# Kernel tuning notes

Measured on AMD Instinct MI355X. Metric: run time of the kernel, lower is better.

## Reference

```python
import jax, jax.numpy as jnp
import numpy as np

D_MODEL, D_STATE, D_CONV, EXPAND = 1024, 16, 4, 2
D_INNER = EXPAND * D_MODEL
BATCH, SEQLEN = 2, 1024


def setup_inputs() -> dict:
    key = jax.random.key(0)
    ks = jax.random.split(key, 8)
    s = lambda fan: 1.0 / np.sqrt(fan)
    x = jax.random.normal(ks[0], (BATCH, SEQLEN, D_MODEL), jnp.float32)
    in_proj_w = jax.random.normal(ks[1], (2 * D_INNER, D_MODEL), jnp.float32) * s(D_MODEL)
    conv_w = jax.random.normal(ks[2], (D_INNER, D_CONV), jnp.float32) * s(D_CONV)
    conv_b = jax.random.normal(ks[3], (D_INNER,), jnp.float32) * 0.02
    x_proj_w = jax.random.normal(ks[4], (2 * D_STATE + 1, D_INNER), jnp.float32) * s(D_INNER)
    dt_proj_w = jax.random.normal(ks[5], (D_INNER, 1), jnp.float32)
    dt_proj_b = jax.random.normal(ks[6], (D_INNER,), jnp.float32) * 0.02
    A_log = jnp.log(jnp.broadcast_to(jnp.arange(1, D_STATE + 1, dtype=jnp.float32), (D_INNER, D_STATE)))
    D_param = jnp.ones((D_INNER,), jnp.float32)
    out_proj_w = jax.random.normal(ks[7], (D_MODEL, D_INNER), jnp.float32) * s(D_INNER)
    return {"x": x, "in_proj_w": in_proj_w, "conv_w": conv_w, "conv_b": conv_b,
            "x_proj_w": x_proj_w, "dt_proj_w": dt_proj_w, "dt_proj_b": dt_proj_b,
            "A_log": A_log, "D_param": D_param, "out_proj_w": out_proj_w}


def reference(x, in_proj_w, conv_w, conv_b, x_proj_w, dt_proj_w, dt_proj_b, A_log, D_param, out_proj_w):
    B, L, _ = x.shape
    d_inner, d_conv = conv_w.shape
    N = A_log.shape[1]

    # in_proj: [B,L,d_model] -> [B,L,2*d_inner], split into ssm branch and gate
    xz = x @ in_proj_w.T
    x_ssm, z = jnp.split(xz, 2, axis=-1)

    # causal depthwise conv1d (padding d_conv-1 on the left, truncated to L)
    xpad = jnp.pad(x_ssm, ((0, 0), (d_conv - 1, 0), (0, 0)))
    xc = conv_b + sum(conv_w[:, k] * xpad[:, k:k + L, :] for k in range(d_conv))
    xc = jax.nn.silu(xc)

    # selective SSM
    A = -jnp.exp(A_log)                                    # [d_inner, N]
    xp = xc @ x_proj_w.T                                   # [B,L,2N+1]
    dt_r, Bv, Cv = xp[..., :1], xp[..., 1:1 + N], xp[..., 1 + N:]
    dt = jax.nn.softplus(dt_r @ dt_proj_w.T + dt_proj_b)   # [B,L,d_inner]
    dA = jnp.exp(dt[..., None] * A)                        # [B,L,d_inner,N]
    dBx = (dt * xc)[..., None] * Bv[:, :, None, :]         # [B,L,d_inner,N]

    def step(h, inputs):
        dA_t, dBx_t, C_t = inputs                          # [B,D,N],[B,D,N],[B,N]
        h = dA_t * h + dBx_t
        y = jnp.einsum('bdn,bn->bd', h, C_t)
        return h, y

    h0 = jnp.zeros((B, d_inner, N), x.dtype)
    xs = (jnp.moveaxis(dA, 1, 0), jnp.moveaxis(dBx, 1, 0), jnp.moveaxis(Cv, 1, 0))
    _, ys = jax.lax.scan(step, h0, xs)                     # ys: [L,B,d_inner]
    y = jnp.moveaxis(ys, 0, 1) + xc * D_param

    y = y * jax.nn.silu(z)
    return y @ out_proj_w.T
```

## Files before the change

### kernel.cpp

```cpp
#include <hip/hip_runtime.h>
#include <hip/hip_bf16.h>
#include <math.h>

#define B_   2
#define L_   1024
#define DM   1024
#define DI   2048
#define NS   16
#define NPJ  33
#define XPW_STRIDE 64
#define NCH  64
#define CHL  16

typedef __bf16 bf16x8 __attribute__((ext_vector_type(8)));
typedef float  f32x4  __attribute__((ext_vector_type(4)));

__device__ __forceinline__ unsigned short f2bf_rn(float x) {
    union { float f; unsigned u; } a; a.f = x;
    unsigned r = a.u + 0x7fffu + ((a.u >> 16) & 1u);
    return (unsigned short)(r >> 16);
}
__device__ __forceinline__ float bf2f(unsigned short h) {
    union { unsigned u; float f; } a; a.u = ((unsigned)h) << 16;
    return a.f;
}
__device__ __forceinline__ float sigmoidf_(float x) { return 1.f / (1.f + __expf(-x)); }
__device__ __forceinline__ float softplusf_(float x) {
    return x > 20.f ? x : log1pf(__expf(x));
}

#define GLDS(g, l) __builtin_amdgcn_global_load_lds( \
    (__attribute__((address_space(1))) void*)(g),    \
    (__attribute__((address_space(3))) void*)(l), 16, 0, 0)

#define XN4   524288
#define W1N4  1048576
#define W2N4  524288
#define WPN4  32768
__global__ __launch_bounds__(256) void cast_all_kernel(
    const float* __restrict__ x, const float* __restrict__ w1,
    const float* __restrict__ w2, const float* __restrict__ xpw,
    unsigned short* __restrict__ xh, unsigned short* __restrict__ xl,
    unsigned short* __restrict__ w1h, unsigned short* __restrict__ w1l,
    unsigned short* __restrict__ w2h, unsigned short* __restrict__ w2l,
    unsigned short* __restrict__ wph, unsigned short* __restrict__ wpl)
{
    int i = blockIdx.x * 256 + threadIdx.x;
    float4 v;
    ushort4 *dh, *dl;
    int li;
    if (i < XN4) {
        li = i; v = ((const float4*)x)[li];
        dh = (ushort4*)xh; dl = (ushort4*)xl;
    } else if (i < XN4 + W1N4) {
        li = i - XN4; v = ((const float4*)w1)[li];
        dh = (ushort4*)w1h; dl = (ushort4*)w1l;
    } else if (i < XN4 + W1N4 + W2N4) {
        li = i - (XN4 + W1N4); v = ((const float4*)w2)[li];
        dh = (ushort4*)w2h; dl = (ushort4*)w2l;
    } else if (i < XN4 + W1N4 + W2N4 + WPN4) {
        li = i - (XN4 + W1N4 + W2N4);
        int j = li >> 9;
        v = (j < NPJ) ? ((const float4*)xpw)[li] : make_float4(0.f, 0.f, 0.f, 0.f);
        dh = (ushort4*)wph; dl = (ushort4*)wpl;
    } else return;
    ushort4 H, L;
    H.x = f2bf_rn(v.x); L.x = f2bf_rn(v.x - bf2f(H.x));
    H.y = f2bf_rn(v.y); L.y = f2bf_rn(v.y - bf2f(H.y));
    H.z = f2bf_rn(v.z); L.z = f2bf_rn(v.z - bf2f(H.z));
    H.w = f2bf_rn(v.w); L.w = f2bf_rn(v.w - bf2f(H.w));
    dh[li] = H; dl[li] = L;
}

template<int BM, int BN, bool AL, bool ATOMIC>
__global__ __launch_bounds__(256) void gemm3_bt(
    const unsigned short* __restrict__ Ah, const unsigned short* __restrict__ Al,
    const unsigned short* __restrict__ Bh, const unsigned short* __restrict__ Bl,
    float* __restrict__ C, int M, int N, int K, int KC)
{
    constexpr int BK = 64;
    constexpr int FM = BM / 32;
    constexpr int FN = BN / 32;
    __shared__ alignas(16) char sAh[BM * BK * 2];
    __shared__ alignas(16) char sAl[AL ? BM * BK * 2 : 16];
    __shared__ alignas(16) char sBh[BN * BK * 2];
    __shared__ alignas(16) char sBl[BN * BK * 2];

    const int tid  = threadIdx.x;
    const int lane = tid & 63;
    const int wave = tid >> 6;
    const int wm = wave >> 1, wn = wave & 1;
    const int m0 = blockIdx.y * BM, n0 = blockIdx.x * BN;
    const int k0 = blockIdx.z * KC;

    f32x4 acc[FM][FN];
#pragma unroll
    for (int i = 0; i < FM; ++i)
#pragma unroll
        for (int j = 0; j < FN; ++j)
            acc[i][j] = (f32x4){0.f, 0.f, 0.f, 0.f};

    for (int kt = k0; kt < k0 + KC; kt += BK) {
#pragma unroll
        for (int iss = 0; iss < BM / 32; ++iss) {
            int o  = (iss * 256 + tid) * 16;
            int r  = o >> 7;
            int cb = (o & 127) ^ ((r & 7) << 4);
            size_t goff = (size_t)(m0 + r) * K + kt + (cb >> 1);
            GLDS(Ah + goff, sAh + iss * 4096 + wave * 1024);
            if (AL) GLDS(Al + goff, sAl + iss * 4096 + wave * 1024);
        }
#pragma unroll
        for (int iss = 0; iss < BN / 32; ++iss) {
            int o  = (iss * 256 + tid) * 16;
            int r  = o >> 7;
            int cb = (o & 127) ^ ((r & 7) << 4);
            size_t goff = (size_t)(n0 + r) * K + kt + (cb >> 1);
            GLDS(Bh + goff, sBh + iss * 4096 + wave * 1024);
            GLDS(Bl + goff, sBl + iss * 4096 + wave * 1024);
        }
        __syncthreads();

#pragma unroll
        for (int kk = 0; kk < 2; ++kk) {
            const int ke = kk * 32 + (lane >> 4) * 8;
            bf16x8 ah[FM], al[FM], bh[FN], bl[FN];
#pragma unroll
            for (int i = 0; i < FM; ++i) {
                int r = wm * (BM / 2) + i * 16 + (lane & 15);
                int off = (r * 128 + ke * 2) ^ ((r & 7) << 4);
                ah[i] = *(const bf16x8*)(sAh + off);
                if (AL) al[i] = *(const bf16x8*)(sAl + off);
            }
#pragma unroll
            for (int j = 0; j < FN; ++j) {
                int r = wn * (BN / 2) + j * 16 + (lane & 15);
                int off = (r * 128 + ke * 2) ^ ((r & 7) << 4);
                bh[j] = *(const bf16x8*)(sBh + off);
                bl[j] = *(const bf16x8*)(sBl + off);
            }
#pragma unroll
            for (int i = 0; i < FM; ++i)
#pragma unroll
                for (int j = 0; j < FN; ++j) {
                    acc[i][j] = __builtin_amdgcn_mfma_f32_16x16x32_bf16(ah[i], bh[j], acc[i][j], 0, 0, 0);
                    acc[i][j] = __builtin_amdgcn_mfma_f32_16x16x32_bf16(ah[i], bl[j], acc[i][j], 0, 0, 0);
                    if (AL) acc[i][j] = __builtin_amdgcn_mfma_f32_16x16x32_bf16(al[i], bh[j], acc[i][j], 0, 0, 0);
                }
        }
        __syncthreads();
    }

    float* Cz = ATOMIC ? C : (C + (size_t)blockIdx.z * M * N);
#pragma unroll
    for (int i = 0; i < FM; ++i)
#pragma unroll
        for (int j = 0; j < FN; ++j) {
            int row = m0 + wm * (BM / 2) + i * 16 + (lane >> 4) * 4;
            int col = n0 + wn * (BN / 2) + j * 16 + (lane & 15);
            float* p = Cz + (size_t)row * N + col;
#pragma unroll
            for (int q = 0; q < 4; ++q) {
                if (ATOMIC) atomicAdd(p + (size_t)q * N, acc[i][j][q]);
                else        p[(size_t)q * N] = acc[i][j][q];
            }
        }
}

__global__ __launch_bounds__(256) void gemm3_xproj(
    const unsigned short* __restrict__ Ah, const unsigned short* __restrict__ Al,
    const unsigned short* __restrict__ Bh, const unsigned short* __restrict__ Bl,
    float* __restrict__ part)
{
    constexpr int BM = 64, BN = 64, BK = 64, KTOT = 2048, KC = 256;
    __shared__ alignas(16) char sAh[BM * 128];
    __shared__ alignas(16) char sAl[BM * 128];
    __shared__ alignas(16) char sBh[BN * 128];
    __shared__ alignas(16) char sBl[BN * 128];

    const int tid  = threadIdx.x;
    const int lane = tid & 63;
    const int wave = tid >> 6;
    const int wm = wave >> 1, wn = wave & 1;
    const int m0 = blockIdx.y * BM;
    const int kt0 = blockIdx.z * KC;

    f32x4 acc[2][2];
#pragma unroll
    for (int i = 0; i < 2; ++i)
#pragma unroll
        for (int j = 0; j < 2; ++j) acc[i][j] = (f32x4){0.f, 0.f, 0.f, 0.f};

    for (int kt = 0; kt < KC; kt += BK) {
#pragma unroll
        for (int iss = 0; iss < 2; ++iss) {
            int o  = (iss * 256 + tid) * 16;
            int r  = o >> 7;
            int cb = (o & 127) ^ ((r & 7) << 4);
            size_t ga = (size_t)(m0 + r) * KTOT + kt0 + kt + (cb >> 1);
            GLDS(Ah + ga, sAh + iss * 4096 + wave * 1024);
            GLDS(Al + ga, sAl + iss * 4096 + wave * 1024);
            size_t gb = (size_t)r * KTOT + kt0 + kt + (cb >> 1);
            GLDS(Bh + gb, sBh + iss * 4096 + wave * 1024);
            GLDS(Bl + gb, sBl + iss * 4096 + wave * 1024);
        }
        __syncthreads();

#pragma unroll
        for (int kk = 0; kk < 2; ++kk) {
            const int ke = kk * 32 + (lane >> 4) * 8;
            bf16x8 ah[2], al[2], bh[2], bl[2];
#pragma unroll
            for (int i = 0; i < 2; ++i) {
                int r = wm * 32 + i * 16 + (lane & 15);
                int off = (r * 128 + ke * 2) ^ ((r & 7) << 4);
                ah[i] = *(const bf16x8*)(sAh + off);
                al[i] = *(const bf16x8*)(sAl + off);
            }
#pragma unroll
            for (int j = 0; j < 2; ++j) {
                int r = wn * 32 + j * 16 + (lane & 15);
                int off = (r * 128 + ke * 2) ^ ((r & 7) << 4);
                bh[j] = *(const bf16x8*)(sBh + off);
                bl[j] = *(const bf16x8*)(sBl + off);
            }
#pragma unroll
            for (int i = 0; i < 2; ++i)
#pragma unroll
                for (int j = 0; j < 2; ++j) {
                    acc[i][j] = __builtin_amdgcn_mfma_f32_16x16x32_bf16(ah[i], bh[j], acc[i][j], 0, 0, 0);
                    acc[i][j] = __builtin_amdgcn_mfma_f32_16x16x32_bf16(ah[i], bl[j], acc[i][j], 0, 0, 0);
                    acc[i][j] = __builtin_amdgcn_mfma_f32_16x16x32_bf16(al[i], bh[j], acc[i][j], 0, 0, 0);
                }
        }
        __syncthreads();
    }

    float* Cp = part + (size_t)blockIdx.z * 2048 * XPW_STRIDE;
#pragma unroll
    for (int i = 0; i < 2; ++i)
#pragma unroll
        for (int j = 0; j < 2; ++j) {
            int row = m0 + wm * 32 + i * 16 + (lane >> 4) * 4;
            int col = wn * 32 + j * 16 + (lane & 15);
            float* p = Cp + (size_t)row * XPW_STRIDE + col;
#pragma unroll
            for (int q = 0; q < 4; ++q) p[(size_t)q * XPW_STRIDE] = acc[i][j][q];
        }
}

__global__ __launch_bounds__(256) void xproj_reduce(
    const float* __restrict__ part, float* __restrict__ xp)
{
    int i = blockIdx.x * 256 + threadIdx.x;
    const float4* p = (const float4*)part;
    float4 s = p[i];
#pragma unroll
    for (int z = 1; z < 8; ++z) {
        float4 v = p[(size_t)z * 32768 + i];
        s.x += v.x; s.y += v.y; s.z += v.z; s.w += v.w;
    }
    ((float4*)xp)[i] = s;
}

__global__ __launch_bounds__(256) void conv_silu_kernel(
    const float* __restrict__ xz, const float* __restrict__ cw,
    const float* __restrict__ cb, unsigned short* __restrict__ xch,
    unsigned short* __restrict__ xcl)
{
    int gid = blockIdx.x * 256 + threadIdx.x;
    int m  = gid >> 9;
    int dv = (gid & 511) << 2;
    int t  = m & (L_ - 1);
    const float* base = xz + (size_t)m * (2 * DI) + dv;
    float4 s  = *(const float4*)(cb + dv);
    float4 w0 = *(const float4*)(cw + (dv + 0) * 4);
    float4 w1 = *(const float4*)(cw + (dv + 1) * 4);
    float4 w2 = *(const float4*)(cw + (dv + 2) * 4);
    float4 w3 = *(const float4*)(cw + (dv + 3) * 4);
    float4 z4 = make_float4(0.f, 0.f, 0.f, 0.f);
    float4 x3 = *(const float4*)(base);
    float4 x2 = (t >= 1) ? *(const float4*)(base - 1 * (2 * DI)) : z4;
    float4 x1 = (t >= 2) ? *(const float4*)(base - 2 * (2 * DI)) : z4;
    float4 x0 = (t >= 3) ? *(const float4*)(base - 3 * (2 * DI)) : z4;
    float r0 = s.x + w0.x * x0.x + w0.y * x1.x + w0.z * x2.x + w0.w * x3.x;
    float r1 = s.y + w1.x * x0.y + w1.y * x1.y + w1.z * x2.y + w1.w * x3.y;
    float r2 = s.z + w2.x * x0.z + w2.y * x1.z + w2.z * x2.z + w2.w * x3.z;
    float r3 = s.w + w3.x * x0.w + w3.y * x1.w + w3.z * x2.w + w3.w * x3.w;
    float4 o;
    o.x = r0 * sigmoidf_(r0);
    o.y = r1 * sigmoidf_(r1);
    o.z = r2 * sigmoidf_(r2);
    o.w = r3 * sigmoidf_(r3);
    ushort4 H, L;
    H.x = f2bf_rn(o.x); L.x = f2bf_rn(o.x - bf2f(H.x));
    H.y = f2bf_rn(o.y); L.y = f2bf_rn(o.y - bf2f(H.y));
    H.z = f2bf_rn(o.z); L.z = f2bf_rn(o.z - bf2f(H.z));
    H.w = f2bf_rn(o.w); L.w = f2bf_rn(o.w - bf2f(H.w));
    *(ushort4*)(xch + (size_t)m * DI + dv) = H;
    *(ushort4*)(xcl + (size_t)m * DI + dv) = L;
}

__global__ __launch_bounds__(256) void scan_pass1(
    const unsigned short* __restrict__ xch, const unsigned short* __restrict__ xcl,
    const float* __restrict__ xp,
    const float* __restrict__ dtw, const float* __restrict__ dtb,
    const float* __restrict__ A_log, float* __restrict__ h0, float* __restrict__ sumdt)
{
    const int b = blockIdx.z, c = blockIdx.y;
    const int tid = threadIdx.x;
    const int d = blockIdx.x * 256 + tid;
    __shared__ float sxp[CHL * XPW_STRIDE];
    const float* xpsrc = xp + (size_t)(b * L_ + c * CHL) * XPW_STRIDE;
    for (int i = tid; i < CHL * XPW_STRIDE / 4; i += 256)
        ((float4*)sxp)[i] = ((const float4*)xpsrc)[i];
    __syncthreads();

    float Av[NS];
#pragma unroll
    for (int n = 0; n < NS; ++n) Av[n] = -__expf(A_log[(size_t)d * NS + n]);
    const float w = dtw[d], bb = dtb[d];
    float h[NS];
#pragma unroll
    for (int n = 0; n < NS; ++n) h[n] = 0.f;
    float sd = 0.f;
    size_t off = (size_t)(b * L_ + c * CHL) * DI + d;

    unsigned short nh = xch[off], nl = xcl[off];
    for (int t = 0; t < CHL; ++t) {
        unsigned short ch = nh, cl = nl;
        nh = xch[off + DI]; nl = xcl[off + DI];
        off += DI;
        float xcv = bf2f(ch) + bf2f(cl);
        float dt  = softplusf_(fmaf(sxp[t * XPW_STRIDE], w, bb));
        sd += dt;
        float u = dt * xcv;
#pragma unroll
        for (int n = 0; n < NS; ++n) {
            float a = __expf(dt * Av[n]);
            h[n] = fmaf(a, h[n], u * sxp[t * XPW_STRIDE + 1 + n]);
        }
    }
    float* hp = h0 + ((size_t)(b * NCH + c) * DI + d) * NS;
#pragma unroll
    for (int n = 0; n < NS; n += 4)
        *(float4*)(hp + n) = make_float4(h[n], h[n + 1], h[n + 2], h[n + 3]);
    sumdt[(size_t)(b * NCH + c) * DI + d] = sd;
}

__global__ __launch_bounds__(256) void scan_pass2(
    const float* __restrict__ A_log, const float* __restrict__ sumdt, float* __restrict__ h0)
{
    int gid = blockIdx.x * 256 + threadIdx.x;
    int b = gid >> 15;
    int r = gid & 32767;
    int d = r >> 4, n = r & 15;
    float An = -__expf(A_log[(size_t)d * NS + n]);
    float h = 0.f;
    for (int c = 0; c < NCH; ++c) {
        size_t idx = ((size_t)(b * NCH + c) * DI + d) * NS + n;
        float hl  = h0[idx];
        float sdv = sumdt[(size_t)(b * NCH + c) * DI + d];
        h0[idx] = h;
        h = fmaf(__expf(An * sdv), h, hl);
    }
}

__global__ __launch_bounds__(256) void scan_pass3(
    const unsigned short* __restrict__ xch, const unsigned short* __restrict__ xcl,
    const float* __restrict__ xp, const float* __restrict__ xz,
    const float* __restrict__ dtw, const float* __restrict__ dtb,
    const float* __restrict__ A_log, const float* __restrict__ Dp,
    const float* __restrict__ hin,
    unsigned short* __restrict__ yh)
{
    const int b = blockIdx.z, c = blockIdx.y;
    const int tid = threadIdx.x;
    const int d = blockIdx.x * 256 + tid;
    __shared__ float sxp[CHL * XPW_STRIDE];
    const float* xpsrc = xp + (size_t)(b * L_ + c * CHL) * XPW_STRIDE;
    for (int i = tid; i < CHL * XPW_STRIDE / 4; i += 256)
        ((float4*)sxp)[i] = ((const float4*)xpsrc)[i];
    __syncthreads();

    float Av[NS];
#pragma unroll
    for (int n = 0; n < NS; ++n) Av[n] = -__expf(A_log[(size_t)d * NS + n]);
    const float w = dtw[d], bb = dtb[d], Dv = Dp[d];
    float h[NS];
    const float* hp = hin + ((size_t)(b * NCH + c) * DI + d) * NS;
#pragma unroll
    for (int n = 0; n < NS; n += 4) {
        float4 v = *(const float4*)(hp + n);
        h[n] = v.x; h[n + 1] = v.y; h[n + 2] = v.z; h[n + 3] = v.w;
    }
    size_t off = (size_t)(b * L_ + c * CHL) * DI + d;
    const float* zp  = xz + (size_t)(b * L_ + c * CHL) * (2 * DI) + DI + d;
    unsigned short* yhp = yh + off;

    unsigned short nh = xch[off], nl = xcl[off];
    float nz = zp[0];
    for (int t = 0; t < CHL; ++t) {
        unsigned short ch = nh, cl = nl;
        float zv = nz;
        nh = xch[off + DI]; nl = xcl[off + DI];
        nz = zp[(size_t)(t + 1) * (2 * DI)];
        off += DI;
        float xcv = bf2f(ch) + bf2f(cl);
        float dt  = softplusf_(fmaf(sxp[t * XPW_STRIDE], w, bb));
        float u = dt * xcv;
        float y = 0.f;
#pragma unroll
        for (int n = 0; n < NS; ++n) {
            float a = __expf(dt * Av[n]);
            h[n] = fmaf(a, h[n], u * sxp[t * XPW_STRIDE + 1 + n]);
            y = fmaf(h[n], sxp[t * XPW_STRIDE + 17 + n], y);
        }
        float out = fmaf(xcv, Dv, y) * (zv * sigmoidf_(zv));
        yhp[(size_t)t * DI] = f2bf_rn(out);
    }
}

extern "C" void kernel_launch(void* const* d_in, const int* in_sizes, int n_in,
                              void* d_out, int out_size, void* d_ws, size_t ws_size,
                              hipStream_t stream)
{
    (void)in_sizes; (void)n_in; (void)out_size;
    const float* x    = (const float*)d_in[0];
    const float* w1   = (const float*)d_in[1];
    const float* cw   = (const float*)d_in[2];
    const float* cb   = (const float*)d_in[3];
    const float* xpw  = (const float*)d_in[4];
    const float* dtw  = (const float*)d_in[5];
    const float* dtb  = (const float*)d_in[6];
    const float* alog = (const float*)d_in[7];
    const float* Dp   = (const float*)d_in[8];
    const float* w2   = (const float*)d_in[9];
    float* out = (float*)d_out;

    char* ws = (char*)d_ws;
    const size_t MB = 1024 * 1024;
    const size_t KB = 1024;
    if (ws_size < 81 * MB) return;

    unsigned short* x_hi  = (unsigned short*)(ws + 0);
    unsigned short* x_lo  = (unsigned short*)(ws + 4 * MB);
    unsigned short* w1_hi = (unsigned short*)(ws + 8 * MB);
    unsigned short* w1_lo = (unsigned short*)(ws + 16 * MB);
    float* xp_part = (float*)(ws + 16 * MB);
    unsigned short* y_hi  = (unsigned short*)(ws + 0);
    float* h0    = (float*)(ws + 8 * MB);
    float* sumdt = (float*)d_out;
    float* xz = (float*)(ws + 24 * MB);
    unsigned short* xc_hi = (unsigned short*)(ws + 56 * MB);
    unsigned short* xc_lo = (unsigned short*)(ws + 64 * MB);
    float* xp = (float*)(ws + 72 * MB);
    unsigned short* wp_hi = (unsigned short*)(ws + 72 * MB + 512 * KB);
    unsigned short* wp_lo = (unsigned short*)(ws + 72 * MB + 768 * KB);
    unsigned short* w2_hi = (unsigned short*)(ws + 73 * MB);
    unsigned short* w2_lo = (unsigned short*)(ws + 77 * MB);

    {
        int total = XN4 + W1N4 + W2N4 + WPN4;
        cast_all_kernel<<<(total + 255) / 256, 256, 0, stream>>>(
            x, w1, w2, xpw, x_hi, x_lo, w1_hi, w1_lo, w2_hi, w2_lo, wp_hi, wp_lo);
    }

    {
        dim3 g(4096 / 128, 2048 / 128, 1);
        gemm3_bt<128, 128, true, false><<<g, 256, 0, stream>>>(x_hi, x_lo, w1_hi, w1_lo, xz, 2048, 4096, 1024, 1024);
    }

    conv_silu_kernel<<<(2048 * 512) / 256, 256, 0, stream>>>(xz, cw, cb, xc_hi, xc_lo);

    {
        dim3 g(1, 2048 / 64, 8);
        gemm3_xproj<<<g, 256, 0, stream>>>(xc_hi, xc_lo, wp_hi, wp_lo, xp_part);
        xproj_reduce<<<128, 256, 0, stream>>>(xp_part, xp);
    }

    {
        dim3 gs(DI / 256, NCH, B_);
        scan_pass1<<<gs, 256, 0, stream>>>(xc_hi, xc_lo, xp, dtw, dtb, alog, h0, sumdt);
        scan_pass2<<<(B_ * DI * NS) / 256, 256, 0, stream>>>(alog, sumdt, h0);
        scan_pass3<<<gs, 256, 0, stream>>>(xc_hi, xc_lo, xp, xz, dtw, dtb, alog, Dp, h0, y_hi);
    }

    {
        hipMemsetAsync(out, 0, (size_t)2048 * 1024 * 4, stream);
        dim3 g(1024 / 128, 2048 / 128, 4);
        gemm3_bt<128, 128, false, true><<<g, 256, 0, stream>>>(y_hi, nullptr, w2_hi, w2_lo, out, 2048, 1024, 2048, 512);
    }
}
```

Measured before the change: 201.7 us.

## Replace atomic split-K output with partial buffers plus reduce, swizzle GEMM workgroups

The out-projection GEMM now writes its split-K partials to a workspace buffer, and a separate float4 reduce kernel sums them into the output. This replaces the memset plus atomicAdd epilogue. GEMM workgroup IDs are remapped with an XCD-aware swizzle (interleaved in groups of 8) so that neighbouring tiles share L2. scan_pass2 batches its loads and exps across 16 chunks to expose memory-level parallelism. The cost is one extra kernel launch and extra traffic for the partial buffers.

```diff
diff --git a/kernel.cpp b/kernel.cpp
--- a/kernel.cpp
+++ b/kernel.cpp
@@ -72,7 +72,7 @@
     dh[li] = H; dl[li] = L;
 }
 
-template<int BM, int BN, bool AL, bool ATOMIC>
+template<int BM, int BN, bool AL>
 __global__ __launch_bounds__(256) void gemm3_bt(
     const unsigned short* __restrict__ Ah, const unsigned short* __restrict__ Al,
     const unsigned short* __restrict__ Bh, const unsigned short* __restrict__ Bl,
@@ -90,7 +90,12 @@
     const int lane = tid & 63;
     const int wave = tid >> 6;
     const int wm = wave >> 1, wn = wave & 1;
-    const int m0 = blockIdx.y * BM, n0 = blockIdx.x * BN;
+
+    int gx = gridDim.x;
+    int nwg = gx * gridDim.y;
+    int wg = blockIdx.y * gx + blockIdx.x;
+    if ((nwg & 7) == 0) wg = (wg & 7) * (nwg >> 3) + (wg >> 3);
+    const int m0 = (wg / gx) * BM, n0 = (wg % gx) * BN;
     const int k0 = blockIdx.z * KC;
 
     f32x4 acc[FM][FN];
@@ -151,7 +156,7 @@
         __syncthreads();
     }
 
-    float* Cz = ATOMIC ? C : (C + (size_t)blockIdx.z * M * N);
+    float* Cz = C + (size_t)blockIdx.z * M * N;
 #pragma unroll
     for (int i = 0; i < FM; ++i)
 #pragma unroll
@@ -160,11 +165,23 @@
             int col = n0 + wn * (BN / 2) + j * 16 + (lane & 15);
             float* p = Cz + (size_t)row * N + col;
 #pragma unroll
-            for (int q = 0; q < 4; ++q) {
-                if (ATOMIC) atomicAdd(p + (size_t)q * N, acc[i][j][q]);
-                else        p[(size_t)q * N] = acc[i][j][q];
-            }
-        }
+            for (int q = 0; q < 4; ++q) p[(size_t)q * N] = acc[i][j][q];
+        }
+}
+
+__global__ __launch_bounds__(256) void reduce4_kernel(
+    const float* __restrict__ part, float* __restrict__ out, int n4, int stride4)
+{
+    int i = blockIdx.x * 256 + threadIdx.x;
+    if (i >= n4) return;
+    const float4* p = (const float4*)part;
+    float4 s = p[i];
+#pragma unroll
+    for (int z = 1; z < 4; ++z) {
+        float4 v = p[(size_t)z * stride4 + i];
+        s.x += v.x; s.y += v.y; s.z += v.z; s.w += v.w;
+    }
+    ((float4*)out)[i] = s;
 }
 
 __global__ __launch_bounds__(256) void gemm3_xproj(
@@ -357,12 +374,22 @@
     int d = r >> 4, n = r & 15;
     float An = -__expf(A_log[(size_t)d * NS + n]);
     float h = 0.f;
-    for (int c = 0; c < NCH; ++c) {
-        size_t idx = ((size_t)(b * NCH + c) * DI + d) * NS + n;
-        float hl  = h0[idx];
-        float sdv = sumdt[(size_t)(b * NCH + c) * DI + d];
-        h0[idx] = h;
-        h = fmaf(__expf(An * sdv), h, hl);
+    for (int cb = 0; cb < NCH; cb += 16) {
+        float hl[16], e[16];
+#pragma unroll
+        for (int j = 0; j < 16; ++j) {
+            size_t ci = (size_t)(b * NCH + cb + j) * DI + d;
+            hl[j] = h0[ci * NS + n];
+            e[j]  = An * sumdt[ci];
+        }
+#pragma unroll
+        for (int j = 0; j < 16; ++j) e[j] = __expf(e[j]);
+#pragma unroll
+        for (int j = 0; j < 16; ++j) {
+            size_t ci = (size_t)(b * NCH + cb + j) * DI + d;
+            h0[ci * NS + n] = h;
+            h = fmaf(e[j], h, hl[j]);
+        }
     }
 }
 
@@ -452,6 +479,7 @@
     float* h0    = (float*)(ws + 8 * MB);
     float* sumdt = (float*)d_out;
     float* xz = (float*)(ws + 24 * MB);
+    float* c_part = (float*)(ws + 24 * MB);
     unsigned short* xc_hi = (unsigned short*)(ws + 56 * MB);
     unsigned short* xc_lo = (unsigned short*)(ws + 64 * MB);
     float* xp = (float*)(ws + 72 * MB);
@@ -468,7 +496,7 @@
 
     {
         dim3 g(4096 / 128, 2048 / 128, 1);
-        gemm3_bt<128, 128, true, false><<<g, 256, 0, stream>>>(x_hi, x_lo, w1_hi, w1_lo, xz, 2048, 4096, 1024, 1024);
+        gemm3_bt<128, 128, true><<<g, 256, 0, stream>>>(x_hi, x_lo, w1_hi, w1_lo, xz, 2048, 4096, 1024, 1024);
     }
 
     conv_silu_kernel<<<(2048 * 512) / 256, 256, 0, stream>>>(xz, cw, cb, xc_hi, xc_lo);
@@ -487,8 +515,8 @@
     }
 
     {
-        hipMemsetAsync(out, 0, (size_t)2048 * 1024 * 4, stream);
         dim3 g(1024 / 128, 2048 / 128, 4);
-        gemm3_bt<128, 128, false, true><<<g, 256, 0, stream>>>(y_hi, nullptr, w2_hi, w2_lo, out, 2048, 1024, 2048, 512);
-    }
-}
+        gemm3_bt<128, 128, false><<<g, 256, 0, stream>>>(y_hi, nullptr, w2_hi, w2_lo, c_part, 2048, 1024, 2048, 512);
+        reduce4_kernel<<<(2048 * 1024 / 4 + 255) / 256, 256, 0, stream>>>(c_part, out, 2048 * 1024 / 4, 2048 * 1024 / 4);
+    }
+}
```

Measured after the change: 184.0 us. -8.7%, faster.
